# Kernel optimization log

Measured on AMD Instinct MI355X. Metric: run time of the kernel, lower is better.

Reference implementation:

```python
import jax, jax.numpy as jnp
import numpy as np
import math

HIDDEN = 1024
N_HEADS = 16
HEAD = HIDDEN // N_HEADS

def setup_inputs() -> dict:
    key = jax.random.key(0)
    k1, k2, k3 = jax.random.split(key, 3)
    encodings = jax.random.normal(k1, (2, 2048, HIDDEN), dtype=jnp.float32)
    W_attn = jax.random.normal(k2, (HIDDEN, 3 * HIDDEN), dtype=jnp.float32) * 0.02
    b_attn = jnp.zeros((3 * HIDDEN,), dtype=jnp.float32)
    W_out = jax.random.normal(k3, (HIDDEN, HIDDEN), dtype=jnp.float32) * 0.02
    b_out = jnp.zeros((HIDDEN,), dtype=jnp.float32)
    return {"encodings": encodings, "W_attn": W_attn, "b_attn": b_attn,
            "W_out": W_out, "b_out": b_out}

def reference(encodings, W_attn, b_attn, W_out, b_out):
    b, n, _ = encodings.shape
    qkv = encodings @ W_attn + b_attn              # [b, n, 3*hidden]
    q, k, v = jnp.split(qkv, 3, axis=-1)
    # 'b n (h l) -> b h n l'
    def to_heads(t):
        return t.reshape(b, n, N_HEADS, HEAD).transpose(0, 2, 1, 3)
    q, k, v = to_heads(q), to_heads(k), to_heads(v)
    # scores[b,h,k,q]; causal mask keeps key_pos <= query_pos
    scores = jnp.einsum('bhki,bhqi->bhkq', k, q) / math.sqrt(HEAD)
    mask = jnp.arange(n)[:, None] <= jnp.arange(n)[None, :]   # [k, q]
    scores = jnp.where(mask, scores, jnp.float32(-10000.0))
    attn = jax.nn.softmax(scores, axis=2)          # softmax over key dim
    combined = jnp.einsum('bhkq,bhkl->bhql', attn, v)  # [b, h, n, head]
    out = combined.transpose(0, 2, 1, 3).reshape(b, n, HIDDEN)
    return out @ W_out + b_out
```

## Files before the change

kernel.cpp:

```cpp
#include <hip/hip_runtime.h>
#include <hip/hip_bf16.h>

typedef __attribute__((ext_vector_type(8))) short bf16x8;
typedef __attribute__((ext_vector_type(4))) short bf16x4;
typedef __attribute__((ext_vector_type(4))) float f32x4;

__device__ __forceinline__ short f2bf(float f) {
    unsigned u = __float_as_uint(f);
    u += 0x7fff + ((u >> 16) & 1);
    return (short)(u >> 16);
}
__device__ __forceinline__ float bf2f(short s) {
    return __uint_as_float(((unsigned)(unsigned short)s) << 16);
}
__device__ __forceinline__ unsigned pk_bf16(float lo, float hi) {
    __hip_bfloat162 t = __float22bfloat162_rn(make_float2(lo, hi));
    unsigned u;
    __builtin_memcpy(&u, &t, 4);
    return u;
}

#define GLOAD_LDS16(gp, lp)                                                            \
    __builtin_amdgcn_global_load_lds(                                                  \
        (const __attribute__((address_space(1))) unsigned*)(gp),                       \
        (__attribute__((address_space(3))) unsigned*)(lp), 16, 0, 0)

#define QK_SCALE 0.180336879f
#define MFMA16(a, b, c) __builtin_amdgcn_mfma_f32_16x16x32_bf16((a), (b), (c), 0, 0, 0)

__device__ __forceinline__ void tcvt_tile(const float* __restrict__ W, short* __restrict__ Wt,
                                          int K, int N, int bx, int by, int t,
                                          short (*tile)[72]) {
    const int k0 = by * 64, n0 = bx * 64;
    #pragma unroll
    for (int jj = 0; jj < 4; ++jj) {
        int row = jj * 16 + (t >> 4);
        int col = (t & 15) * 4;
        f32x4 v = *(const f32x4*)&W[(size_t)(k0 + row) * N + n0 + col];
        bf16x4 b = {f2bf(v.x), f2bf(v.y), f2bf(v.z), f2bf(v.w)};
        *(bf16x4*)&tile[row][col] = b;
    }
    __syncthreads();
    const int nr = t >> 2, kc = (t & 3) * 16;
    bf16x8 o0, o1;
    #pragma unroll
    for (int j = 0; j < 8; ++j) { o0[j] = tile[kc + j][nr]; o1[j] = tile[kc + 8 + j][nr]; }
    short* dst = &Wt[(size_t)(n0 + nr) * K + k0 + kc];
    *(bf16x8*)dst = o0;
    *(bf16x8*)(dst + 8) = o1;
}

__global__ __launch_bounds__(256) void prep_kernel(
    const float* __restrict__ enc, const float* __restrict__ Wa,
    const float* __restrict__ ba, const float* __restrict__ Wo,
    const float* __restrict__ bo, short* __restrict__ Abf,
    short* __restrict__ WtA, short* __restrict__ bbA,
    short* __restrict__ WtO, short* __restrict__ bbO)
{
    __shared__ alignas(16) short tile[64][72];
    const int id = blockIdx.x, t = threadIdx.x;
    if (id < 2048) {
        const int i = id * 2048 + t * 8;
        f32x4 a = *(const f32x4*)&enc[i];
        f32x4 b = *(const f32x4*)&enc[i + 4];
        bf16x8 o = {f2bf(a.x), f2bf(a.y), f2bf(a.z), f2bf(a.w),
                    f2bf(b.x), f2bf(b.y), f2bf(b.z), f2bf(b.w)};
        *(bf16x8*)&Abf[i] = o;
    } else if (id == 2048) {
        for (int j = t * 8; j < 3072; j += 2048) {
            f32x4 a = *(const f32x4*)&ba[j];
            f32x4 b = *(const f32x4*)&ba[j + 4];
            bf16x8 o = {f2bf(a.x), f2bf(a.y), f2bf(a.z), f2bf(a.w),
                        f2bf(b.x), f2bf(b.y), f2bf(b.z), f2bf(b.w)};
            *(bf16x8*)&bbA[j] = o;
        }
    } else if (id == 2049) {
        if (t < 128) {
            const int j = t * 8;
            f32x4 a = *(const f32x4*)&bo[j];
            f32x4 b = *(const f32x4*)&bo[j + 4];
            bf16x8 o = {f2bf(a.x), f2bf(a.y), f2bf(a.z), f2bf(a.w),
                        f2bf(b.x), f2bf(b.y), f2bf(b.z), f2bf(b.w)};
            *(bf16x8*)&bbO[j] = o;
        }
        __syncthreads();
    } else if (id < 2818) {
        const int lid = id - 2050;
        tcvt_tile(Wa, WtA, 1024, 3072, lid % 48, lid / 48, t, tile);
    } else {
        const int lid = id - 2818;
        tcvt_tile(Wo, WtO, 1024, 1024, lid % 16, lid / 16, t, tile);
    }
}

template<int BN, bool F32OUT, bool SPLIT3>
__global__ __launch_bounds__(256) void gemm_bt(
    const short* __restrict__ A, const short* __restrict__ Bt,
    const short* __restrict__ bias, void* __restrict__ C,
    short* __restrict__ Kw, short* __restrict__ Vw, int M, int N, int K)
{
    __shared__ alignas(16) short As[128 * 32];
    __shared__ alignas(16) short Bs[BN * 32];
    __shared__ alignas(16) short Ct[SPLIT3 ? 128 * 128 : 1];

    const int tid = threadIdx.x, w = tid >> 6, lane = tid & 63;
    const int quad = lane >> 4, l16 = lane & 15;
    constexpr int MT = (BN == 128) ? 4 : 2;
    const int wm = (BN == 128) ? (w >> 1) : w;
    const int wn = (BN == 128) ? (w & 1) : 0;
    const int m0 = blockIdx.y * 128, n0 = blockIdx.x * BN;
    const int srow = lane >> 2, scol = (lane & 3) * 8;

    f32x4 acc[MT][4] = {};

    for (int k0 = 0; k0 < K; k0 += 32) {
        __syncthreads();
        #pragma unroll
        for (int jj = 0; jj < 2; ++jj) {
            const int rb = w * 32 + jj * 16;
            GLOAD_LDS16(&A[(size_t)(m0 + rb + srow) * K + k0 + scol], &As[rb * 32]);
        }
        if (BN == 128) {
            #pragma unroll
            for (int jj = 0; jj < 2; ++jj) {
                const int rb = w * 32 + jj * 16;
                GLOAD_LDS16(&Bt[(size_t)(n0 + rb + srow) * K + k0 + scol], &Bs[rb * 32]);
            }
        } else {
            const int rb = w * 16;
            GLOAD_LDS16(&Bt[(size_t)(n0 + rb + srow) * K + k0 + scol], &Bs[rb * 32]);
        }
        __syncthreads();
        bf16x8 af[MT], bfr[4];
        #pragma unroll
        for (int i = 0; i < MT; ++i)
            af[i] = *(const bf16x8*)&As[(wm * (MT * 16) + i * 16 + l16) * 32 + quad * 8];
        #pragma unroll
        for (int i = 0; i < 4; ++i)
            bfr[i] = *(const bf16x8*)&Bs[(wn * 64 + i * 16 + l16) * 32 + quad * 8];
        #pragma unroll
        for (int mt = 0; mt < MT; ++mt)
            #pragma unroll
            for (int nt = 0; nt < 4; ++nt)
                acc[mt][nt] = MFMA16(af[mt], bfr[nt], acc[mt][nt]);
    }

    if (SPLIT3) {
        const int g = n0 >> 10;
        const int lc0 = n0 & 1023;
        if (g < 2) {
            #pragma unroll
            for (int nt = 0; nt < 4; ++nt) {
                const int col = wn * 64 + nt * 16 + l16;
                const float bv = bf2f(bias[n0 + col]);
                const int chunk = col >> 3, wi = col & 7;
                #pragma unroll
                for (int mt = 0; mt < 4; ++mt) {
                    const int rbase = wm * 64 + mt * 16 + quad * 4;
                    #pragma unroll
                    for (int r = 0; r < 4; ++r) {
                        const int row = rbase + r;
                        float v = acc[mt][nt][r] + bv;
                        if (g == 0) v *= QK_SCALE;
                        Ct[row * 128 + (((chunk ^ (row & 15)) << 3) | wi)] = f2bf(v);
                    }
                }
            }
        } else {
            #pragma unroll
            for (int nt = 0; nt < 4; ++nt) {
                const int d = wn * 64 + nt * 16 + l16;
                const float bv = bf2f(bias[n0 + d]);
                const int dsw = d & 15;
                #pragma unroll
                for (int mt = 0; mt < 4; ++mt) {
                    const int key0 = wm * 64 + mt * 16 + quad * 4;
                    bf16x4 p = {f2bf(acc[mt][nt][0] + bv), f2bf(acc[mt][nt][1] + bv),
                                f2bf(acc[mt][nt][2] + bv), f2bf(acc[mt][nt][3] + bv)};
                    *(bf16x4*)&Ct[d * 128 + ((((key0 >> 3) ^ dsw) << 3) | (key0 & 7))] = p;
                }
            }
        }
        __syncthreads();
        const int batch = m0 >> 11;
        const int kc0 = (m0 & 2047) >> 6;
        const int head0 = lc0 >> 6;
        if (g == 0) {
            short* dst = (short*)C;
            #pragma unroll
            for (int i = 0; i < 8; ++i) {
                const int idx = i * 256 + tid;
                const int row = idx >> 4, chunk = idx & 15;
                bf16x8 v = *(const bf16x8*)&Ct[row * 128 + ((chunk ^ (row & 15)) << 3)];
                *(bf16x8*)&dst[(size_t)(m0 + row) * 1024 + lc0 + chunk * 8] = v;
            }
        } else if (g == 1) {
            #pragma unroll
            for (int i = 0; i < 8; ++i) {
                const int idx = i * 256 + tid;
                const int qd = idx >> 9, c = idx & 511;
                const int kcL = qd >> 1, headL = qd & 1;
                const int s = c >> 7, h2 = (c >> 6) & 1;
                const int l16c = c & 15, quadc = (c >> 4) & 3;
                const int row = kcL * 64 + s * 16 + l16c;
                const int colc = headL * 8 + h2 * 4 + quadc;
                bf16x8 v = *(const bf16x8*)&Ct[row * 128 + ((colc ^ (row & 15)) << 3)];
                const int bh = batch * 16 + head0 + headL, kc = kc0 + kcL;
                *(bf16x8*)&Kw[((size_t)(bh * 32 + kc) * 512 + c) * 8] = v;
            }
        } else {
            #pragma unroll
            for (int i = 0; i < 8; ++i) {
                const int idx = i * 256 + tid;
                const int qd = idx >> 9, c = idx & 511;
                const int kcL = qd >> 1, headL = qd & 1;
                const int h2 = c >> 8, dt = (c >> 6) & 3;
                const int l16c = c & 15, quadc = (c >> 4) & 3;
                const int d = headL * 64 + dt * 16 + l16c;
                const int keyc = kcL * 8 + h2 * 4 + quadc;
                bf16x8 v = *(const bf16x8*)&Ct[d * 128 + ((keyc ^ (d & 15)) << 3)];
                const int bh = batch * 16 + head0 + headL, kc = kc0 + kcL;
                *(bf16x8*)&Vw[((size_t)(bh * 32 + kc) * 512 + c) * 8] = v;
            }
        }
    } else {
        #pragma unroll
        for (int nt = 0; nt < 4; ++nt) {
            const int col = n0 + wn * 64 + nt * 16 + l16;
            const float bv = bf2f(bias[col]);
            #pragma unroll
            for (int mt = 0; mt < MT; ++mt) {
                const int row = m0 + wm * (MT * 16) + mt * 16 + quad * 4;
                #pragma unroll
                for (int r = 0; r < 4; ++r) {
                    float v = acc[mt][nt][r] + bv;
                    if (F32OUT) ((float*)C)[(size_t)(row + r) * N + col] = v;
                    else        ((short*)C)[(size_t)(row + r) * N + col] = f2bf(v);
                }
            }
        }
    }
}

__global__ __launch_bounds__(256) void attn_kernel(
    const short* __restrict__ Qw, const short* __restrict__ Kx,
    const short* __restrict__ Vx, short* __restrict__ comb)
{
    __shared__ alignas(16) short Ps[4][2][16 * 72];
    __shared__ alignas(16) float cbuf[2][2][64][16];
    __shared__ float clacc[2][2][64];

    const int tid = threadIdx.x, w4 = tid >> 6, lane = tid & 63;
    const int w = w4 & 1;
    const int h = w4 >> 1;
    const int quad = lane >> 4, l16 = lane & 15;
    const int bh = blockIdx.x;
    const int tA = blockIdx.y, tB = 63 - tA;
    const int batch = bh >> 4, head = bh & 15;
    const size_t rowbase = (size_t)batch * 2048;
    const int hcol = head * 64;
    const int q0A = tA * 32 + w * 16, q0B = tB * 32 + w * 16;
    const int diagA = tA >> 1, diagB = tB >> 1;
    const short* Kxbh = Kx + (size_t)bh * 131072;
    const short* Vxbh = Vx + (size_t)bh * 131072;
    const int lofs = lane * 8;
    short* pwA = &Ps[w4][0][0];
    short* pwB = &Ps[w4][1][0];

    bf16x8 qfA[2], qfB[2];
    {
        const short* pa = &Qw[(rowbase + q0A + l16) * 1024 + hcol];
        const short* pb = &Qw[(rowbase + q0B + l16) * 1024 + hcol];
        qfA[0] = *(const bf16x8*)(pa + quad * 8);
        qfA[1] = *(const bf16x8*)(pa + 32 + quad * 8);
        qfB[0] = *(const bf16x8*)(pb + quad * 8);
        qfB[1] = *(const bf16x8*)(pb + 32 + quad * 8);
    }

    f32x4 otA[4] = {}, otB[4] = {};
    float laccA = 0.f, laccB = 0.f;

    bf16x8 kf[4][2];
    {
        const short* kb0 = Kxbh + (size_t)h * 4096;
        #pragma unroll
        for (int s = 0; s < 4; ++s) {
            kf[s][0] = *(const bf16x8*)&kb0[(s * 2 + 0) * 512 + lofs];
            kf[s][1] = *(const bf16x8*)&kb0[(s * 2 + 1) * 512 + lofs];
        }
    }

    for (int kc = h; kc <= diagB; kc += 2) {
        const bool actA = (kc <= diagA);
        const int key0 = kc * 64;

        const short* vb = Vxbh + (size_t)kc * 4096;
        bf16x8 vf[2][4];
        #pragma unroll
        for (int hh = 0; hh < 2; ++hh)
            #pragma unroll
            for (int dt = 0; dt < 4; ++dt)
                vf[hh][dt] = *(const bf16x8*)&vb[(hh * 4 + dt) * 512 + lofs];

        f32x4 svA[4], svB[4];
        #pragma unroll
        for (int s = 0; s < 4; ++s) {
            f32x4 a = {0.f, 0.f, 0.f, 0.f};
            a = MFMA16(kf[s][0], qfB[0], a);
            a = MFMA16(kf[s][1], qfB[1], a);
            svB[s] = a;
            if (actA) {
                f32x4 b = {0.f, 0.f, 0.f, 0.f};
                b = MFMA16(kf[s][0], qfA[0], b);
                b = MFMA16(kf[s][1], qfA[1], b);
                svA[s] = b;
            }
        }

        if (kc + 2 <= diagB) {
            const short* kb = Kxbh + (size_t)(kc + 2) * 4096;
            #pragma unroll
            for (int s = 0; s < 4; ++s) {
                kf[s][0] = *(const bf16x8*)&kb[(s * 2 + 0) * 512 + lofs];
                kf[s][1] = *(const bf16x8*)&kb[(s * 2 + 1) * 512 + lofs];
            }
        }

        if (kc == diagB) {
            const int qq = q0B + l16;
            #pragma unroll
            for (int s = 0; s < 4; ++s) {
                const int keyb = key0 + s * 16 + quad * 4;
                #pragma unroll
                for (int r = 0; r < 4; ++r)
                    svB[s][r] = (keyb + r <= qq) ? svB[s][r] : -1e30f;
            }
        }
        #pragma unroll
        for (int s = 0; s < 4; ++s) {
            #pragma unroll
            for (int r = 0; r < 4; ++r) svB[s][r] = exp2f(svB[s][r]);
            laccB += (svB[s][0] + svB[s][1]) + (svB[s][2] + svB[s][3]);
            *(unsigned*)&pwB[l16 * 72 + s * 16 + quad * 4]     = pk_bf16(svB[s][0], svB[s][1]);
            *(unsigned*)&pwB[l16 * 72 + s * 16 + quad * 4 + 2] = pk_bf16(svB[s][2], svB[s][3]);
        }
        if (actA) {
            if (kc == diagA) {
                const int qq = q0A + l16;
                #pragma unroll
                for (int s = 0; s < 4; ++s) {
                    const int keyb = key0 + s * 16 + quad * 4;
                    #pragma unroll
                    for (int r = 0; r < 4; ++r)
                        svA[s][r] = (keyb + r <= qq) ? svA[s][r] : -1e30f;
                }
            }
            #pragma unroll
            for (int s = 0; s < 4; ++s) {
                #pragma unroll
                for (int r = 0; r < 4; ++r) svA[s][r] = exp2f(svA[s][r]);
                laccA += (svA[s][0] + svA[s][1]) + (svA[s][2] + svA[s][3]);
                *(unsigned*)&pwA[l16 * 72 + s * 16 + quad * 4]     = pk_bf16(svA[s][0], svA[s][1]);
                *(unsigned*)&pwA[l16 * 72 + s * 16 + quad * 4 + 2] = pk_bf16(svA[s][2], svA[s][3]);
            }
        }

        {
            bf16x8 pfB0 = *(const bf16x8*)&pwB[l16 * 72 + quad * 8];
            bf16x8 pfB1 = *(const bf16x8*)&pwB[l16 * 72 + 32 + quad * 8];
            #pragma unroll
            for (int dt = 0; dt < 4; ++dt) {
                otB[dt] = MFMA16(vf[0][dt], pfB0, otB[dt]);
                otB[dt] = MFMA16(vf[1][dt], pfB1, otB[dt]);
            }
            if (actA) {
                bf16x8 pfA0 = *(const bf16x8*)&pwA[l16 * 72 + quad * 8];
                bf16x8 pfA1 = *(const bf16x8*)&pwA[l16 * 72 + 32 + quad * 8];
                #pragma unroll
                for (int dt = 0; dt < 4; ++dt) {
                    otA[dt] = MFMA16(vf[0][dt], pfA0, otA[dt]);
                    otA[dt] = MFMA16(vf[1][dt], pfA1, otA[dt]);
                }
            }
        }
    }

    __syncthreads();
    if (h == 1) {
        #pragma unroll
        for (int dt = 0; dt < 4; ++dt) {
            *(f32x4*)&cbuf[w][0][lane][dt * 4] = otA[dt];
            *(f32x4*)&cbuf[w][1][lane][dt * 4] = otB[dt];
        }
        clacc[w][0][lane] = laccA;
        clacc[w][1][lane] = laccB;
    }
    __syncthreads();
    if (h == 0) {
        #pragma unroll
        for (int dt = 0; dt < 4; ++dt) {
            otA[dt] += *(const f32x4*)&cbuf[w][0][lane][dt * 4];
            otB[dt] += *(const f32x4*)&cbuf[w][1][lane][dt * 4];
        }
        laccA += clacc[w][0][lane];
        laccB += clacc[w][1][lane];

        laccA += __shfl_xor(laccA, 16);
        laccA += __shfl_xor(laccA, 32);
        laccB += __shfl_xor(laccB, 16);
        laccB += __shfl_xor(laccB, 32);
        const float invA = 1.0f / laccA, invB = 1.0f / laccB;

        #pragma unroll
        for (int dt = 0; dt < 4; ++dt) {
            *(unsigned*)&pwA[l16 * 72 + dt * 16 + quad * 4]     = pk_bf16(otA[dt][0] * invA, otA[dt][1] * invA);
            *(unsigned*)&pwA[l16 * 72 + dt * 16 + quad * 4 + 2] = pk_bf16(otA[dt][2] * invA, otA[dt][3] * invA);
            *(unsigned*)&pwB[l16 * 72 + dt * 16 + quad * 4]     = pk_bf16(otB[dt][0] * invB, otB[dt][1] * invB);
            *(unsigned*)&pwB[l16 * 72 + dt * 16 + quad * 4 + 2] = pk_bf16(otB[dt][2] * invB, otB[dt][3] * invB);
        }
        {
            const int qr = lane >> 2, dc = (lane & 3) * 16;
            bf16x8 a0 = *(const bf16x8*)&pwA[qr * 72 + dc];
            bf16x8 a1 = *(const bf16x8*)&pwA[qr * 72 + dc + 8];
            short* dstA = &comb[(rowbase + q0A + qr) * 1024 + hcol + dc];
            *(bf16x8*)dstA = a0;
            *(bf16x8*)(dstA + 8) = a1;
            bf16x8 b0 = *(const bf16x8*)&pwB[qr * 72 + dc];
            bf16x8 b1 = *(const bf16x8*)&pwB[qr * 72 + dc + 8];
            short* dstB = &comb[(rowbase + q0B + qr) * 1024 + hcol + dc];
            *(bf16x8*)dstB = b0;
            *(bf16x8*)(dstB + 8) = b1;
        }
    }
}

extern "C" void kernel_launch(void* const* d_in, const int* in_sizes, int n_in,
                              void* d_out, int out_size, void* d_ws, size_t ws_size,
                              hipStream_t stream)
{
    const float* enc = (const float*)d_in[0];
    const float* Wa  = (const float*)d_in[1];
    const float* ba  = (const float*)d_in[2];
    const float* Wo  = (const float*)d_in[3];
    const float* bo  = (const float*)d_in[4];
    float* out = (float*)d_out;

    char* ws = (char*)d_ws;
    short* Abf  = (short*)ws;
    short* comb = (short*)ws;
    short* WtO  = (short*)(ws + ((size_t)8 << 20));
    short* bbA  = (short*)(ws + ((size_t)10 << 20));
    short* bbO  = (short*)(ws + ((size_t)10 << 20) + 16384);
    short* WtA  = (short*)(ws + ((size_t)11 << 20));
    short* Kx   = (short*)(ws + ((size_t)17 << 20));
    short* Vx   = (short*)(ws + ((size_t)25 << 20));
    short* Qw   = (short*)(ws + ((size_t)33 << 20));

    prep_kernel<<<3074, 256, 0, stream>>>(enc, Wa, ba, Wo, bo, Abf, WtA, bbA, WtO, bbO);
    gemm_bt<128, false, true><<<dim3(24, 32), 256, 0, stream>>>(
        Abf, WtA, bbA, Qw, Kx, Vx, 4096, 3072, 1024);
    attn_kernel<<<dim3(32, 32), 256, 0, stream>>>(Qw, Kx, Vx, comb);
    gemm_bt<64, true, false><<<dim3(16, 32), 256, 0, stream>>>(
        comb, WtO, bbO, out, nullptr, nullptr, 4096, 1024, 1024);
}
```

Measured before the change: 201.6 us.

## Double GEMM K-step to 64 with XOR-swizzled LDS tiles and aliased epilogue buffer

Each main-loop iteration of the bf16 GEMM now stages a 64-wide K slice instead of 32, which halves the number of barrier pairs per tile. The LDS layout uses an XOR swizzle on 16-byte chunks to avoid bank conflicts on the MFMA fragment reads. The epilogue staging buffer Ct now aliases the A/B staging area, with an added barrier, to keep total LDS use down. The larger LDS footprint per block may reduce occupancy, and loads are still not double-buffered.

```diff
diff --git a/kernel.cpp b/kernel.cpp
--- a/kernel.cpp
+++ b/kernel.cpp
@@ -99,9 +99,10 @@
     const short* __restrict__ bias, void* __restrict__ C,
     short* __restrict__ Kw, short* __restrict__ Vw, int M, int N, int K)
 {
-    __shared__ alignas(16) short As[128 * 32];
-    __shared__ alignas(16) short Bs[BN * 32];
-    __shared__ alignas(16) short Ct[SPLIT3 ? 128 * 128 : 1];
+    __shared__ alignas(16) short LB[128 * 64 + BN * 64];
+    short* As = LB;
+    short* Bs = LB + 128 * 64;
+    short* Ct = LB;
 
     const int tid = threadIdx.x, w = tid >> 6, lane = tid & 63;
     const int quad = lane >> 4, l16 = lane & 15;
@@ -109,45 +110,58 @@
     const int wm = (BN == 128) ? (w >> 1) : w;
     const int wn = (BN == 128) ? (w & 1) : 0;
     const int m0 = blockIdx.y * 128, n0 = blockIdx.x * BN;
-    const int srow = lane >> 2, scol = (lane & 3) * 8;
+    const int srow = lane >> 3;
+    const int scol = ((lane & 7) ^ srow) * 8;
 
     f32x4 acc[MT][4] = {};
 
-    for (int k0 = 0; k0 < K; k0 += 32) {
+    for (int k0 = 0; k0 < K; k0 += 64) {
         __syncthreads();
         #pragma unroll
-        for (int jj = 0; jj < 2; ++jj) {
-            const int rb = w * 32 + jj * 16;
-            GLOAD_LDS16(&A[(size_t)(m0 + rb + srow) * K + k0 + scol], &As[rb * 32]);
+        for (int jj = 0; jj < 4; ++jj) {
+            const int rb = w * 32 + jj * 8;
+            GLOAD_LDS16(&A[(size_t)(m0 + rb + srow) * K + k0 + scol], &As[rb * 64]);
         }
         if (BN == 128) {
             #pragma unroll
+            for (int jj = 0; jj < 4; ++jj) {
+                const int rb = w * 32 + jj * 8;
+                GLOAD_LDS16(&Bt[(size_t)(n0 + rb + srow) * K + k0 + scol], &Bs[rb * 64]);
+            }
+        } else {
+            #pragma unroll
             for (int jj = 0; jj < 2; ++jj) {
-                const int rb = w * 32 + jj * 16;
-                GLOAD_LDS16(&Bt[(size_t)(n0 + rb + srow) * K + k0 + scol], &Bs[rb * 32]);
-            }
-        } else {
-            const int rb = w * 16;
-            GLOAD_LDS16(&Bt[(size_t)(n0 + rb + srow) * K + k0 + scol], &Bs[rb * 32]);
+                const int rb = w * 16 + jj * 8;
+                GLOAD_LDS16(&Bt[(size_t)(n0 + rb + srow) * K + k0 + scol], &Bs[rb * 64]);
+            }
         }
         __syncthreads();
-        bf16x8 af[MT], bfr[4];
-        #pragma unroll
-        for (int i = 0; i < MT; ++i)
-            af[i] = *(const bf16x8*)&As[(wm * (MT * 16) + i * 16 + l16) * 32 + quad * 8];
-        #pragma unroll
-        for (int i = 0; i < 4; ++i)
-            bfr[i] = *(const bf16x8*)&Bs[(wn * 64 + i * 16 + l16) * 32 + quad * 8];
-        #pragma unroll
-        for (int mt = 0; mt < MT; ++mt)
-            #pragma unroll
-            for (int nt = 0; nt < 4; ++nt)
-                acc[mt][nt] = MFMA16(af[mt], bfr[nt], acc[mt][nt]);
+        #pragma unroll
+        for (int half = 0; half < 2; ++half) {
+            const int kc2 = half * 4 + quad;
+            bf16x8 af[MT], bfr[4];
+            #pragma unroll
+            for (int i = 0; i < MT; ++i) {
+                const int row = wm * (MT * 16) + i * 16 + l16;
+                af[i] = *(const bf16x8*)&As[row * 64 + ((kc2 ^ (row & 7)) << 3)];
+            }
+            #pragma unroll
+            for (int i = 0; i < 4; ++i) {
+                const int row = wn * 64 + i * 16 + l16;
+                bfr[i] = *(const bf16x8*)&Bs[row * 64 + ((kc2 ^ (row & 7)) << 3)];
+            }
+            #pragma unroll
+            for (int mt = 0; mt < MT; ++mt)
+                #pragma unroll
+                for (int nt = 0; nt < 4; ++nt)
+                    acc[mt][nt] = MFMA16(af[mt], bfr[nt], acc[mt][nt]);
+        }
     }
 
     if (SPLIT3) {
         const int g = n0 >> 10;
         const int lc0 = n0 & 1023;
+        __syncthreads();
         if (g < 2) {
             #pragma unroll
             for (int nt = 0; nt < 4; ++nt) {
```

Result: faster. 187.5 us (-7.0%).
